# Optimization experiments

Hardware: AMD Instinct MI355X
Metric: run time of the kernel (lower is better)

Reference implementation:

```python
import jax, jax.numpy as jnp
import numpy as np

N_NODES = 50000
N_EDGES = 800000
D = 128
BN_EPS = 1e-5


def _bn(x, gamma, beta):
    # BatchNorm1d in training mode: biased batch stats over node axis
    m = jnp.mean(x, axis=0)
    v = jnp.mean((x - m) ** 2, axis=0)
    return gamma * (x - m) * jax.lax.rsqrt(v + BN_EPS) + beta


def setup_inputs() -> dict:
    key = jax.random.key(0)
    ks = jax.random.split(key, 8)
    feats = jax.random.normal(ks[0], (N_NODES, D), dtype=jnp.float32)
    src = jax.random.randint(ks[1], (N_EDGES,), 0, N_NODES, dtype=jnp.int32)
    dst = jax.random.randint(ks[2], (N_EDGES,), 0, N_NODES, dtype=jnp.int32)
    s = 1.0 / np.sqrt(D)
    W1 = jax.random.uniform(ks[3], (D, D), jnp.float32, -s, s)
    b1 = jax.random.uniform(ks[4], (D,), jnp.float32, -s, s)
    W2 = jax.random.uniform(ks[5], (D, D), jnp.float32, -s, s)
    b2 = jax.random.uniform(ks[6], (D,), jnp.float32, -s, s)
    ones = jnp.ones((D,), jnp.float32)
    zeros = jnp.zeros((D,), jnp.float32)
    return {
        "feats": feats, "src": src, "dst": dst,
        "W1": W1, "b1": b1, "g1": ones, "be1": zeros,
        "W2": W2, "b2": b2, "g2": ones, "be2": zeros,
        "g3": ones, "be3": zeros,
    }


def reference(feats, src, dst, W1, b1, g1, be1, W2, b2, g2, be2, g3, be3):
    # GIN 'max' aggregation: for each dst node, elementwise max over source feats
    msgs = feats[src]  # [E, D] gather (memory-bound)
    agg = jax.ops.segment_max(msgs, dst, num_segments=N_NODES)
    # DGL gives 0 for nodes with no in-edges; segment_max gives -inf
    agg = jnp.where(jnp.isfinite(agg), agg, 0.0)
    h = feats + agg  # (1 + eps) * feats + agg, eps = 0
    # GINNodeFunc: Linear -> BN -> ReLU -> Linear -> BN -> ReLU
    h = jax.nn.relu(_bn(h @ W1 + b1, g1, be1))
    h = jax.nn.relu(_bn(h @ W2 + b2, g2, be2))
    # outer BN; dropout treated as identity (eval / deterministic baseline)
    return _bn(h, g3, be3)
```

## Files before the change

kernel.cpp:

```cpp
#include <hip/hip_runtime.h>
#include <stdint.h>


#define NN 50000
#define NE 800000
#define DD 128
#define BN_EPS 1e-5f
#define NB 1563
#define CAPB 768
#define NBK 64
#define EPB 12500

typedef short bf16x8 __attribute__((ext_vector_type(8)));
typedef float f32x4 __attribute__((ext_vector_type(4)));

__device__ __forceinline__ float bf2f(unsigned short u) {
    return __uint_as_float(((unsigned int)u) << 16);
}
__device__ __forceinline__ unsigned short f2bf(float f) {
    unsigned int u = __float_as_uint(f);
    u += 0x7fffu + ((u >> 16) & 1u);
    return (unsigned short)(u >> 16);
}
__device__ __forceinline__ float plo(unsigned int p) { return bf2f((unsigned short)(p & 0xffffu)); }
__device__ __forceinline__ float phi(unsigned int p) { return bf2f((unsigned short)(p >> 16)); }
__device__ __forceinline__ unsigned int encf(float f) {
    unsigned int b = __float_as_uint(f);
    return (b & 0x80000000u) ? ~b : (b | 0x80000000u);
}
__device__ __forceinline__ float decf(unsigned int e) {
    return __uint_as_float((e & 0x80000000u) ? (e ^ 0x80000000u) : ~e);
}

__global__ __launch_bounds__(256) void k_prep(
    const float* __restrict__ feats, unsigned int* __restrict__ fb,
    const float* __restrict__ W1, const float* __restrict__ W2,
    unsigned short* __restrict__ Wt1, unsigned short* __restrict__ Wt2,
    unsigned int* __restrict__ bcur)
{
    int g = blockIdx.x * 256 + threadIdx.x;
    float4 v = *reinterpret_cast<const float4*>(feats + (size_t)g * 4);
    uint2 o;
    o.x = (unsigned int)f2bf(v.x) | ((unsigned int)f2bf(v.y) << 16);
    o.y = (unsigned int)f2bf(v.z) | ((unsigned int)f2bf(v.w) << 16);
    *reinterpret_cast<uint2*>(fb + (size_t)g * 2) = o;
    if (g < 16384) {
        int row = g >> 7, col = g & 127;
        Wt1[col * DD + row] = f2bf(W1[g]);
    } else if (g < 32768) {
        int h = g - 16384;
        int row = h >> 7, col = h & 127;
        Wt2[col * DD + row] = f2bf(W2[h]);
    }
    if (g < NB) bcur[(size_t)g * 16] = (unsigned int)g * CAPB;
}

__global__ __launch_bounds__(1024) void k_bin(
    const int* __restrict__ src, const int* __restrict__ dst,
    unsigned int* __restrict__ bcur, unsigned int* __restrict__ tmp)
{
    __shared__ unsigned int words[EPB];
    __shared__ unsigned short loff[EPB];
    __shared__ unsigned int lhist[NB];
    __shared__ unsigned int lbase[NB];
    int tid = threadIdx.x;
    int e0 = blockIdx.x * EPB;
    for (int c = tid; c < NB; c += 1024) lhist[c] = 0u;
    __syncthreads();
    for (int i = tid; i < EPB; i += 1024) {
        int d = dst[e0 + i];
        int s = src[e0 + i];
        words[i] = ((unsigned int)s << 16) | (unsigned int)d;
        loff[i] = (unsigned short)atomicAdd(&lhist[d >> 5], 1u);
    }
    __syncthreads();
    for (int c = tid; c < NB; c += 1024) {
        unsigned int cnt = lhist[c];
        lbase[c] = cnt ? atomicAdd(&bcur[(size_t)c * 16], cnt) : 0u;
    }
    __syncthreads();
    for (int i = tid; i < EPB; i += 1024) {
        unsigned int w = words[i];
        int b = (int)((w & 0xffffu) >> 5);
        unsigned int pos = lbase[b] + (unsigned int)loff[i];
        if (pos < (unsigned int)(b + 1) * CAPB) tmp[pos] = w;
    }
}

__global__ __launch_bounds__(512) void k_aggmax(
    const unsigned int* __restrict__ F,
    const unsigned int* __restrict__ tmp,
    const unsigned int* __restrict__ bcur,
    unsigned int* __restrict__ h0)
{
    __shared__ unsigned int mx[32 * 128];
    int tid = threadIdx.x;
    int b = blockIdx.x;
    int n0 = b * 32;
    for (int i = tid; i < 32 * 128; i += 512) mx[i] = 0u;
    __syncthreads();

    int wave = tid >> 6, lane = tid & 63;
    unsigned int base = (unsigned int)b * CAPB;
    unsigned int cnt = bcur[(size_t)b * 16] - base;
    if (cnt > CAPB) cnt = CAPB;

    for (unsigned int start = (unsigned int)wave * 64; start < cnt; start += 512) {
        int nw = (int)(cnt - start) < 64 ? (int)(cnt - start) : 64;
        unsigned int pw = (lane < nw) ? tmp[base + start + lane] : 0u;
        int j = 0;
        for (; j + 8 <= nw; j += 8) {
            unsigned int e0 = __shfl(pw, j + 0);
            unsigned int e1 = __shfl(pw, j + 1);
            unsigned int e2 = __shfl(pw, j + 2);
            unsigned int e3 = __shfl(pw, j + 3);
            unsigned int e4 = __shfl(pw, j + 4);
            unsigned int e5 = __shfl(pw, j + 5);
            unsigned int e6 = __shfl(pw, j + 6);
            unsigned int e7 = __shfl(pw, j + 7);
            unsigned int u0 = F[(e0 >> 16) * 64 + lane];
            unsigned int u1 = F[(e1 >> 16) * 64 + lane];
            unsigned int u2 = F[(e2 >> 16) * 64 + lane];
            unsigned int u3 = F[(e3 >> 16) * 64 + lane];
            unsigned int u4 = F[(e4 >> 16) * 64 + lane];
            unsigned int u5 = F[(e5 >> 16) * 64 + lane];
            unsigned int u6 = F[(e6 >> 16) * 64 + lane];
            unsigned int u7 = F[(e7 >> 16) * 64 + lane];
            int d0 = (e0 & 31) << 7, d1 = (e1 & 31) << 7;
            int d2 = (e2 & 31) << 7, d3 = (e3 & 31) << 7;
            int d4 = (e4 & 31) << 7, d5 = (e5 & 31) << 7;
            int d6 = (e6 & 31) << 7, d7 = (e7 & 31) << 7;
            atomicMax(&mx[d0 + lane], encf(plo(u0)));
            atomicMax(&mx[d0 + 64 + lane], encf(phi(u0)));
            atomicMax(&mx[d1 + lane], encf(plo(u1)));
            atomicMax(&mx[d1 + 64 + lane], encf(phi(u1)));
            atomicMax(&mx[d2 + lane], encf(plo(u2)));
            atomicMax(&mx[d2 + 64 + lane], encf(phi(u2)));
            atomicMax(&mx[d3 + lane], encf(plo(u3)));
            atomicMax(&mx[d3 + 64 + lane], encf(phi(u3)));
            atomicMax(&mx[d4 + lane], encf(plo(u4)));
            atomicMax(&mx[d4 + 64 + lane], encf(phi(u4)));
            atomicMax(&mx[d5 + lane], encf(plo(u5)));
            atomicMax(&mx[d5 + 64 + lane], encf(phi(u5)));
            atomicMax(&mx[d6 + lane], encf(plo(u6)));
            atomicMax(&mx[d6 + 64 + lane], encf(phi(u6)));
            atomicMax(&mx[d7 + lane], encf(plo(u7)));
            atomicMax(&mx[d7 + 64 + lane], encf(phi(u7)));
        }
        for (; j < nw; ++j) {
            unsigned int e = __shfl(pw, j);
            unsigned int u = F[(e >> 16) * 64 + lane];
            int d = (e & 31) << 7;
            atomicMax(&mx[d + lane], encf(plo(u)));
            atomicMax(&mx[d + 64 + lane], encf(phi(u)));
        }
    }
    __syncthreads();

    for (int idx2 = tid; idx2 < 32 * 64; idx2 += 512) {
        int node = idx2 >> 6, j = idx2 & 63;
        int n = n0 + node;
        if (n >= NN) continue;
        unsigned int e0 = mx[node * 128 + j];
        unsigned int e1 = mx[node * 128 + 64 + j];
        float m0 = (e0 == 0u) ? 0.f : decf(e0);
        float m1 = (e1 == 0u) ? 0.f : decf(e1);
        unsigned int pf = F[n * 64 + j];
        h0[n * 64 + j] = (unsigned int)f2bf(plo(pf) + m0) |
                         ((unsigned int)f2bf(phi(pf) + m1) << 16);
    }
}

template <int FUSE>
__global__ __launch_bounds__(512) void k_gemm(
    const unsigned short* __restrict__ X, const unsigned short* __restrict__ Wt,
    const float* __restrict__ bias, const float* __restrict__ pa,
    const float* __restrict__ pc, unsigned short* __restrict__ Y,
    float* __restrict__ partials)
{
    __shared__ float lsum[128], lsq[128];
    int tid = threadIdx.x;
    if (tid < 128) { lsum[tid] = 0.f; lsq[tid] = 0.f; }
    __syncthreads();
    int wave = tid >> 6, lane = tid & 63;
    int quad = lane >> 4, l16 = lane & 15;
    int m0 = blockIdx.x * 64 + (wave >> 1) * 16;
    int nh = (wave & 1) * 64;
    int myrow = m0 + l16;
    int kq = quad * 8;

    f32x4 acc[4];
#pragma unroll
    for (int j = 0; j < 4; ++j)
#pragma unroll
        for (int r = 0; r < 4; ++r) acc[j][r] = 0.f;

#pragma unroll
    for (int k0 = 0; k0 < 128; k0 += 32) {
        bf16x8 a;
        if (myrow < NN) {
            a = *reinterpret_cast<const bf16x8*>(X + myrow * DD + k0 + kq);
            if (FUSE) {
                float4 av0 = *reinterpret_cast<const float4*>(pa + k0 + kq);
                float4 av1 = *reinterpret_cast<const float4*>(pa + k0 + kq + 4);
                float4 cv0 = *reinterpret_cast<const float4*>(pc + k0 + kq);
                float4 cv1 = *reinterpret_cast<const float4*>(pc + k0 + kq + 4);
                float fa[8] = {av0.x, av0.y, av0.z, av0.w, av1.x, av1.y, av1.z, av1.w};
                float fc[8] = {cv0.x, cv0.y, cv0.z, cv0.w, cv1.x, cv1.y, cv1.z, cv1.w};
#pragma unroll
                for (int j = 0; j < 8; ++j) {
                    float v = fmaxf(fa[j] * bf2f((unsigned short)a[j]) + fc[j], 0.f);
                    a[j] = (short)f2bf(v);
                }
            }
        } else {
#pragma unroll
            for (int j = 0; j < 8; ++j) a[j] = 0;
        }
#pragma unroll
        for (int j = 0; j < 4; ++j) {
            bf16x8 bb = *reinterpret_cast<const bf16x8*>(Wt + (nh + j * 16 + l16) * DD + k0 + kq);
            acc[j] = __builtin_amdgcn_mfma_f32_16x16x32_bf16(a, bb, acc[j], 0, 0, 0);
        }
    }

    int rbase = m0 + quad * 4;
#pragma unroll
    for (int j = 0; j < 4; ++j) {
        int col = nh + j * 16 + l16;
        float bcol = bias[col];
        float s = 0.f, q = 0.f;
#pragma unroll
        for (int r = 0; r < 4; ++r) {
            int row = rbase + r;
            if (row < NN) {
                float v = acc[j][r] + bcol;
                Y[row * DD + col] = f2bf(v);
                s += v;
                q += v * v;
            }
        }
        s += __shfl_xor(s, 16, 64);
        s += __shfl_xor(s, 32, 64);
        q += __shfl_xor(q, 16, 64);
        q += __shfl_xor(q, 32, 64);
        if (quad == 0) {
            atomicAdd(&lsum[col], s);
            atomicAdd(&lsq[col], q);
        }
    }
    __syncthreads();
    if (tid < 128) {
        partials[blockIdx.x * 256 + tid] = lsum[tid];
        partials[blockIdx.x * 256 + 128 + tid] = lsq[tid];
    }
}

__global__ void k_redparams(const float* __restrict__ partials, int nblk,
                            const float* __restrict__ g, const float* __restrict__ be,
                            float* __restrict__ a, float* __restrict__ c) {
    __shared__ float ls[256], lq[256];
    int t = threadIdx.x;
    int col = blockIdx.x;
    float s = 0.f, q = 0.f;
    for (int i = t; i < nblk; i += 256) {
        s += partials[i * 256 + col];
        q += partials[i * 256 + 128 + col];
    }
    ls[t] = s; lq[t] = q;
    __syncthreads();
    for (int off = 128; off > 0; off >>= 1) {
        if (t < off) { ls[t] += ls[t + off]; lq[t] += lq[t + off]; }
        __syncthreads();
    }
    if (t == 0) {
        float mean = ls[0] / (float)NN;
        float var = fmaxf(lq[0] / (float)NN - mean * mean, 0.f);
        float av = g[col] * rsqrtf(var + BN_EPS);
        a[col] = av;
        c[col] = be[col] - mean * av;
    }
}

__global__ __launch_bounds__(256) void k_zstats(
    const unsigned short* __restrict__ Y2, const float* __restrict__ a2,
    const float* __restrict__ c2, float* __restrict__ partials)
{
    __shared__ float ls[256], lq[256];
    int t = threadIdx.x;
    int col = t & 127, half = t >> 7;
    float av = a2[col], cv = c2[col];
    float s = 0.f, q = 0.f;
    for (int row = blockIdx.x * 2 + half; row < NN; row += gridDim.x * 2) {
        float z = fmaxf(av * bf2f(Y2[row * DD + col]) + cv, 0.f);
        s += z;
        q += z * z;
    }
    ls[t] = s;
    lq[t] = q;
    __syncthreads();
    if (t < 128) {
        partials[blockIdx.x * 256 + t] = ls[t] + ls[t + 128];
        partials[blockIdx.x * 256 + 128 + t] = lq[t] + lq[t + 128];
    }
}

__global__ __launch_bounds__(256) void k_out(
    const unsigned short* __restrict__ Y2, const float* __restrict__ a2,
    const float* __restrict__ c2, const float* __restrict__ a3,
    const float* __restrict__ c3, float* __restrict__ out)
{
    int g = blockIdx.x * 256 + threadIdx.x;
    int base = g * 4;
    int c0 = base & 127;
    uint2 p = *reinterpret_cast<const uint2*>(Y2 + base);
    float4 av2 = *reinterpret_cast<const float4*>(a2 + c0);
    float4 cv2 = *reinterpret_cast<const float4*>(c2 + c0);
    float4 av3 = *reinterpret_cast<const float4*>(a3 + c0);
    float4 cv3 = *reinterpret_cast<const float4*>(c3 + c0);
    float z0 = fmaxf(av2.x * plo(p.x) + cv2.x, 0.f);
    float z1 = fmaxf(av2.y * phi(p.x) + cv2.y, 0.f);
    float z2 = fmaxf(av2.z * plo(p.y) + cv2.z, 0.f);
    float z3 = fmaxf(av2.w * phi(p.y) + cv2.w, 0.f);
    float4 o;
    o.x = av3.x * z0 + cv3.x;
    o.y = av3.y * z1 + cv3.y;
    o.z = av3.z * z2 + cv3.z;
    o.w = av3.w * z3 + cv3.w;
    *reinterpret_cast<float4*>(out + base) = o;
}

extern "C" void kernel_launch(void* const* d_in, const int* in_sizes, int n_in,
                              void* d_out, int out_size, void* d_ws, size_t ws_size,
                              hipStream_t stream) {
    (void)in_sizes; (void)n_in; (void)out_size; (void)ws_size;
    const float* feats = (const float*)d_in[0];
    const int* src = (const int*)d_in[1];
    const int* dst = (const int*)d_in[2];
    const float* W1 = (const float*)d_in[3];
    const float* b1 = (const float*)d_in[4];
    const float* g1 = (const float*)d_in[5];
    const float* be1 = (const float*)d_in[6];
    const float* W2 = (const float*)d_in[7];
    const float* b2 = (const float*)d_in[8];
    const float* g2 = (const float*)d_in[9];
    const float* be2 = (const float*)d_in[10];
    const float* g3 = (const float*)d_in[11];
    const float* be3 = (const float*)d_in[12];
    float* out = (float*)d_out;

    char* p = (char*)d_ws;
    auto alloc = [&](size_t n) { char* r = p; p += (n + 255) & ~(size_t)255; return r; };
    unsigned int* fb = (unsigned int*)alloc((size_t)NN * 64 * 4);
    unsigned int* h0 = (unsigned int*)alloc((size_t)NN * 64 * 4);
    unsigned int* bcur = (unsigned int*)alloc((size_t)NB * 16 * 4);
    unsigned int* tmp = (unsigned int*)alloc((size_t)NB * CAPB * 4);
    unsigned short* Y1 = (unsigned short*)alloc((size_t)NN * DD * 2);
    unsigned short* Y2 = (unsigned short*)alloc((size_t)NN * DD * 2);
    unsigned short* Wt1 = (unsigned short*)alloc((size_t)DD * DD * 2);
    unsigned short* Wt2 = (unsigned short*)alloc((size_t)DD * DD * 2);
    float* partials = (float*)alloc((size_t)784 * 256 * 4);
    float* a1 = (float*)alloc(DD * 4); float* c1 = (float*)alloc(DD * 4);
    float* a2 = (float*)alloc(DD * 4); float* c2 = (float*)alloc(DD * 4);
    float* a3 = (float*)alloc(DD * 4); float* c3 = (float*)alloc(DD * 4);

    k_prep<<<6250, 256, 0, stream>>>(feats, fb, W1, W2, Wt1, Wt2, bcur);
    k_bin<<<NBK, 1024, 0, stream>>>(src, dst, bcur, tmp);
    k_aggmax<<<NB, 512, 0, stream>>>(fb, tmp, bcur, h0);
    k_gemm<0><<<782, 512, 0, stream>>>((const unsigned short*)h0, Wt1, b1,
                                       nullptr, nullptr, Y1, partials);
    k_redparams<<<128, 256, 0, stream>>>(partials, 782, g1, be1, a1, c1);
    k_gemm<1><<<782, 512, 0, stream>>>(Y1, Wt2, b2, a1, c1, Y2, partials);
    k_redparams<<<128, 256, 0, stream>>>(partials, 782, g2, be2, a2, c2);
    k_zstats<<<256, 256, 0, stream>>>(Y2, a2, c2, partials);
    k_redparams<<<128, 256, 0, stream>>>(partials, 256, g3, be3, a3, c3);
    k_out<<<6250, 256, 0, stream>>>(Y2, a2, c2, a3, c3, out);
}
```

Before: 261.9 us.

## Replace LDS atomicMax aggregation with in-block counting sort and register max

The max-aggregation kernel no longer does two shared-memory atomicMax operations per edge per lane. Each block now counting-sorts its bucketed edges by destination node in LDS, and each wave walks the edge list of its 4 nodes, reducing the max in registers with fmaxf. This removes LDS atomic contention and the float-to-ordered-int encode/decode. In exchange it adds a histogram pass, a serial prefix sum and extra barriers, and load balance now depends on per-node degree, so waves whose nodes have many edges finish last. The per-block edge cap stays, since each thread holds at most two edge words in registers.

```diff
diff --git a/kernel.cpp b/kernel.cpp
--- a/kernel.cpp
+++ b/kernel.cpp
@@ -24,13 +24,6 @@
 }
 __device__ __forceinline__ float plo(unsigned int p) { return bf2f((unsigned short)(p & 0xffffu)); }
 __device__ __forceinline__ float phi(unsigned int p) { return bf2f((unsigned short)(p >> 16)); }
-__device__ __forceinline__ unsigned int encf(float f) {
-    unsigned int b = __float_as_uint(f);
-    return (b & 0x80000000u) ? ~b : (b | 0x80000000u);
-}
-__device__ __forceinline__ float decf(unsigned int e) {
-    return __uint_as_float((e & 0x80000000u) ? (e ^ 0x80000000u) : ~e);
-}
 
 __global__ __launch_bounds__(256) void k_prep(
     const float* __restrict__ feats, unsigned int* __restrict__ fb,
@@ -93,81 +86,65 @@
     const unsigned int* __restrict__ bcur,
     unsigned int* __restrict__ h0)
 {
-    __shared__ unsigned int mx[32 * 128];
+    __shared__ unsigned int sorted[CAPB];
+    __shared__ unsigned int hist[32];
+    __shared__ unsigned int hbase[33];
     int tid = threadIdx.x;
     int b = blockIdx.x;
+    if (tid < 32) hist[tid] = 0u;
+    __syncthreads();
+    unsigned int rb = (unsigned int)b * CAPB;
+    unsigned int cnt = bcur[(size_t)b * 16] - rb;
+    if (cnt > CAPB) cnt = CAPB;
+
+    unsigned int wreg[2]; unsigned short lo[2]; int nw = 0;
+    for (unsigned int i = tid; i < cnt; i += 512) {
+        unsigned int ww = tmp[rb + i];
+        wreg[nw] = ww;
+        lo[nw] = (unsigned short)atomicAdd(&hist[ww & 31], 1u);
+        nw++;
+    }
+    __syncthreads();
+    if (tid == 0) {
+        unsigned int acc = 0;
+#pragma unroll
+        for (int i = 0; i < 32; ++i) { hbase[i] = acc; acc += hist[i]; }
+        hbase[32] = acc;
+    }
+    __syncthreads();
+    for (int k = 0; k < nw; ++k)
+        sorted[hbase[wreg[k] & 31] + (unsigned int)lo[k]] = wreg[k];
+    __syncthreads();
+
+    int wave = tid >> 6, lane = tid & 63;
     int n0 = b * 32;
-    for (int i = tid; i < 32 * 128; i += 512) mx[i] = 0u;
-    __syncthreads();
-
-    int wave = tid >> 6, lane = tid & 63;
-    unsigned int base = (unsigned int)b * CAPB;
-    unsigned int cnt = bcur[(size_t)b * 16] - base;
-    if (cnt > CAPB) cnt = CAPB;
-
-    for (unsigned int start = (unsigned int)wave * 64; start < cnt; start += 512) {
-        int nw = (int)(cnt - start) < 64 ? (int)(cnt - start) : 64;
-        unsigned int pw = (lane < nw) ? tmp[base + start + lane] : 0u;
-        int j = 0;
-        for (; j + 8 <= nw; j += 8) {
-            unsigned int e0 = __shfl(pw, j + 0);
-            unsigned int e1 = __shfl(pw, j + 1);
-            unsigned int e2 = __shfl(pw, j + 2);
-            unsigned int e3 = __shfl(pw, j + 3);
-            unsigned int e4 = __shfl(pw, j + 4);
-            unsigned int e5 = __shfl(pw, j + 5);
-            unsigned int e6 = __shfl(pw, j + 6);
-            unsigned int e7 = __shfl(pw, j + 7);
-            unsigned int u0 = F[(e0 >> 16) * 64 + lane];
-            unsigned int u1 = F[(e1 >> 16) * 64 + lane];
-            unsigned int u2 = F[(e2 >> 16) * 64 + lane];
-            unsigned int u3 = F[(e3 >> 16) * 64 + lane];
-            unsigned int u4 = F[(e4 >> 16) * 64 + lane];
-            unsigned int u5 = F[(e5 >> 16) * 64 + lane];
-            unsigned int u6 = F[(e6 >> 16) * 64 + lane];
-            unsigned int u7 = F[(e7 >> 16) * 64 + lane];
-            int d0 = (e0 & 31) << 7, d1 = (e1 & 31) << 7;
-            int d2 = (e2 & 31) << 7, d3 = (e3 & 31) << 7;
-            int d4 = (e4 & 31) << 7, d5 = (e5 & 31) << 7;
-            int d6 = (e6 & 31) << 7, d7 = (e7 & 31) << 7;
-            atomicMax(&mx[d0 + lane], encf(plo(u0)));
-            atomicMax(&mx[d0 + 64 + lane], encf(phi(u0)));
-            atomicMax(&mx[d1 + lane], encf(plo(u1)));
-            atomicMax(&mx[d1 + 64 + lane], encf(phi(u1)));
-            atomicMax(&mx[d2 + lane], encf(plo(u2)));
-            atomicMax(&mx[d2 + 64 + lane], encf(phi(u2)));
-            atomicMax(&mx[d3 + lane], encf(plo(u3)));
-            atomicMax(&mx[d3 + 64 + lane], encf(phi(u3)));
-            atomicMax(&mx[d4 + lane], encf(plo(u4)));
-            atomicMax(&mx[d4 + 64 + lane], encf(phi(u4)));
-            atomicMax(&mx[d5 + lane], encf(plo(u5)));
-            atomicMax(&mx[d5 + 64 + lane], encf(phi(u5)));
-            atomicMax(&mx[d6 + lane], encf(plo(u6)));
-            atomicMax(&mx[d6 + 64 + lane], encf(phi(u6)));
-            atomicMax(&mx[d7 + lane], encf(plo(u7)));
-            atomicMax(&mx[d7 + 64 + lane], encf(phi(u7)));
-        }
-        for (; j < nw; ++j) {
-            unsigned int e = __shfl(pw, j);
-            unsigned int u = F[(e >> 16) * 64 + lane];
-            int d = (e & 31) << 7;
-            atomicMax(&mx[d + lane], encf(plo(u)));
-            atomicMax(&mx[d + 64 + lane], encf(phi(u)));
-        }
-    }
-    __syncthreads();
-
-    for (int idx2 = tid; idx2 < 32 * 64; idx2 += 512) {
-        int node = idx2 >> 6, j = idx2 & 63;
-        int n = n0 + node;
+#pragma unroll 1
+    for (int dd = wave * 4; dd < wave * 4 + 4; ++dd) {
+        int n = n0 + dd;
         if (n >= NN) continue;
-        unsigned int e0 = mx[node * 128 + j];
-        unsigned int e1 = mx[node * 128 + 64 + j];
-        float m0 = (e0 == 0u) ? 0.f : decf(e0);
-        float m1 = (e1 == 0u) ? 0.f : decf(e1);
-        unsigned int pf = F[n * 64 + j];
-        h0[n * 64 + j] = (unsigned int)f2bf(plo(pf) + m0) |
-                         ((unsigned int)f2bf(phi(pf) + m1) << 16);
+        int st = (int)hbase[dd], en = (int)hbase[dd + 1];
+        float m0 = -3.0e38f, m1 = -3.0e38f;
+        int i = st;
+        for (; i + 4 <= en; i += 4) {
+            unsigned int w0 = sorted[i], w1 = sorted[i + 1];
+            unsigned int w2 = sorted[i + 2], w3 = sorted[i + 3];
+            unsigned int u0 = F[(w0 >> 16) * 64 + lane];
+            unsigned int u1 = F[(w1 >> 16) * 64 + lane];
+            unsigned int u2 = F[(w2 >> 16) * 64 + lane];
+            unsigned int u3 = F[(w3 >> 16) * 64 + lane];
+            m0 = fmaxf(m0, fmaxf(fmaxf(plo(u0), plo(u1)), fmaxf(plo(u2), plo(u3))));
+            m1 = fmaxf(m1, fmaxf(fmaxf(phi(u0), phi(u1)), fmaxf(phi(u2), phi(u3))));
+        }
+        for (; i < en; ++i) {
+            unsigned int ww = sorted[i];
+            unsigned int u = F[(ww >> 16) * 64 + lane];
+            m0 = fmaxf(m0, plo(u));
+            m1 = fmaxf(m1, phi(u));
+        }
+        if (en == st) { m0 = 0.f; m1 = 0.f; }
+        unsigned int pf = F[n * 64 + lane];
+        h0[n * 64 + lane] = (unsigned int)f2bf(plo(pf) + m0) |
+                            ((unsigned int)f2bf(phi(pf) + m1) << 16);
     }
 }
 
```

After: 258.5 us. About the same (-1.3%).
